# Optimization experiments

Hardware: AMD Instinct MI355X
Metric: run time of the kernel (lower is better)

## Reference

```python
import jax, jax.numpy as jnp
import numpy as np

RANK_WEIGHT = 0.1  # init kwarg rank_weight
EPS = 1e-08


def setup_inputs() -> dict:
    key = jax.random.key(0)
    k1, k2, k3, k4 = jax.random.split(key, 4)
    B, D = 8192, 128
    return {
        "q_embeddings": jax.random.normal(k1, (B, D), dtype=jnp.float32),
        "a_embeddings": jax.random.normal(k2, (B, D), dtype=jnp.float32),
        "question_ids": jax.random.randint(k3, (B,), 0, 2048, dtype=jnp.int64),
        "ranks": jax.random.uniform(k4, (B,), dtype=jnp.float32),
    }


def reference(q_embeddings, a_embeddings, question_ids, ranks):
    # NOTE: the original computes q@a.T/temperature into `similarity` but the
    # per-sample loop recomputes sims WITHOUT temperature; we match the loop math.
    sims = jnp.matmul(q_embeddings, a_embeddings.T)  # [B, B]
    same_q = question_ids[:, None] == question_ids[None, :]  # [B, B] bool
    # pos_mask weight per positive column j: 1 - rank_weight * ranks[j]
    w = jnp.where(same_q, 1.0 - RANK_WEIGHT * ranks[None, :], 0.0)  # [B, B]
    # stable exp-ratio: sum(w*exp(s)) / sum(exp(s))
    m = jnp.max(sims, axis=1, keepdims=True)
    e = jnp.exp(sims - m)
    num = jnp.sum(w * e, axis=1)
    den = jnp.sum(e, axis=1)
    loss = jnp.mean(-jnp.log(num / den + EPS))
    pred = jnp.argmax(sims, axis=1)  # [B]
    correct = jnp.take_along_axis(w, pred[:, None], axis=1)[:, 0] > 0
    accuracy = jnp.mean(correct.astype(jnp.float32))
    return loss, accuracy
```

## Files before the change

kernel.cpp:

```cpp
#include <hip/hip_runtime.h>
#include <hip/hip_bf16.h>
#include <cmath>

#define B_N 8192
#define D_K 128
#define CSPLIT 8
#define T_ITERS 16

typedef short bf16x8 __attribute__((ext_vector_type(8)));
typedef unsigned short u16x8 __attribute__((ext_vector_type(8)));
typedef float f32x4  __attribute__((ext_vector_type(4)));

__device__ inline unsigned short f2bf(float f) {
    unsigned u = __builtin_bit_cast(unsigned, f);
    u += 0x7fffu + ((u >> 16) & 1u);
    return (unsigned short)(u >> 16);
}

__global__ void cvt_kernel(const float* __restrict__ q, const float* __restrict__ a,
                           unsigned short* __restrict__ qb, unsigned short* __restrict__ ab,
                           float* __restrict__ out) {
    int g = blockIdx.x * blockDim.x + threadIdx.x;
    if (g < 2) out[g] = 0.0f;
    float4 q0 = reinterpret_cast<const float4*>(q)[g * 2];
    float4 q1 = reinterpret_cast<const float4*>(q)[g * 2 + 1];
    u16x8 oq;
    oq[0] = f2bf(q0.x); oq[1] = f2bf(q0.y); oq[2] = f2bf(q0.z); oq[3] = f2bf(q0.w);
    oq[4] = f2bf(q1.x); oq[5] = f2bf(q1.y); oq[6] = f2bf(q1.z); oq[7] = f2bf(q1.w);
    *reinterpret_cast<u16x8*>(qb + (size_t)g * 8) = oq;

    float4 a0 = reinterpret_cast<const float4*>(a)[g * 2];
    float4 a1 = reinterpret_cast<const float4*>(a)[g * 2 + 1];
    u16x8 oa;
    oa[0] = f2bf(a0.x); oa[1] = f2bf(a0.y); oa[2] = f2bf(a0.z); oa[3] = f2bf(a0.w);
    oa[4] = f2bf(a1.x); oa[5] = f2bf(a1.y); oa[6] = f2bf(a1.z); oa[7] = f2bf(a1.w);
    const int col = g >> 4, sq = g & 15, s = sq >> 2, quad = sq & 3;
    const int chunk = ((col >> 4) * 4 + s) * 64 + quad * 16 + (col & 15);
    *reinterpret_cast<u16x8*>(ab + (size_t)chunk * 8) = oa;
}

__launch_bounds__(256, 4)
__global__ void mpl_part_kernel(const unsigned short* __restrict__ qb,
                                const unsigned short* __restrict__ ab,
                                const int* __restrict__ qids,
                                const float* __restrict__ ranks,
                                float* __restrict__ pden, float* __restrict__ pnum,
                                float* __restrict__ pmax, float* __restrict__ pmaxp) {
    const int tid  = threadIdx.x;
    const int lane = tid & 63;
    const int wave = tid >> 6;
    const int rg   = blockIdx.x >> 3;
    const int cs   = blockIdx.x & 7;
    const int rowBase = rg * 32;
    const int quad = lane >> 4;
    const int l15  = lane & 15;

    bf16x8 qfrag[2][4];
    #pragma unroll
    for (int rt = 0; rt < 2; ++rt) {
        const unsigned short* qrow = qb + (size_t)(rowBase + rt * 16 + l15) * D_K + quad * 8;
        #pragma unroll
        for (int s = 0; s < 4; ++s)
            qfrag[rt][s] = *reinterpret_cast<const bf16x8*>(qrow + s * 32);
    }

    int qidrow[2][4];
    #pragma unroll
    for (int rt = 0; rt < 2; ++rt)
        #pragma unroll
        for (int r = 0; r < 4; ++r)
            qidrow[rt][r] = qids[rowBase + rt * 16 + quad * 4 + r];

    float den[2][4], num[2][4], mxv[2][4], mxp[2][4];
    #pragma unroll
    for (int rt = 0; rt < 2; ++rt)
        #pragma unroll
        for (int r = 0; r < 4; ++r) {
            den[rt][r] = 0.f; num[rt][r] = 0.f;
            mxv[rt][r] = -INFINITY; mxp[rt][r] = -INFINITY;
        }

    const float L2E = 1.4426950408889634f;
    const float CB  = 64.0f;

    const int colStart = cs * 1024 + wave * 256;
    const int tileBase = colStart >> 4;

    #pragma unroll 2
    for (int t = 0; t < T_ITERS; ++t) {
        const int c  = colStart + t * 16 + l15;
        const int qc = qids[c];
        const float wc = 1.0f - 0.1f * ranks[c];

        const unsigned short* bbase = ab + ((size_t)(tileBase + t) * 4) * 512 + lane * 8;
        bf16x8 bfrag[4];
        #pragma unroll
        for (int s = 0; s < 4; ++s)
            bfrag[s] = *reinterpret_cast<const bf16x8*>(bbase + s * 512);

        f32x4 acc0 = {0.f, 0.f, 0.f, 0.f};
        f32x4 acc1 = {0.f, 0.f, 0.f, 0.f};
        #pragma unroll
        for (int s = 0; s < 4; ++s) {
            acc0 = __builtin_amdgcn_mfma_f32_16x16x32_bf16(qfrag[0][s], bfrag[s], acc0, 0, 0, 0);
            acc1 = __builtin_amdgcn_mfma_f32_16x16x32_bf16(qfrag[1][s], bfrag[s], acc1, 0, 0, 0);
        }

        #pragma unroll
        for (int r = 0; r < 4; ++r) {
            {
                float sv = acc0[r];
                float e  = __builtin_amdgcn_exp2f(fmaf(sv, L2E, -CB));
                bool pos = (qc == qidrow[0][r]);
                den[0][r] += e;
                num[0][r] = fmaf(pos ? wc : 0.0f, e, num[0][r]);
                mxv[0][r] = fmaxf(mxv[0][r], sv);
                mxp[0][r] = fmaxf(mxp[0][r], pos ? sv : -INFINITY);
            }
            {
                float sv = acc1[r];
                float e  = __builtin_amdgcn_exp2f(fmaf(sv, L2E, -CB));
                bool pos = (qc == qidrow[1][r]);
                den[1][r] += e;
                num[1][r] = fmaf(pos ? wc : 0.0f, e, num[1][r]);
                mxv[1][r] = fmaxf(mxv[1][r], sv);
                mxp[1][r] = fmaxf(mxp[1][r], pos ? sv : -INFINITY);
            }
        }
    }

    #pragma unroll
    for (int m = 1; m <= 8; m <<= 1) {
        #pragma unroll
        for (int rt = 0; rt < 2; ++rt)
            #pragma unroll
            for (int r = 0; r < 4; ++r) {
                den[rt][r] += __shfl_xor(den[rt][r], m, 64);
                num[rt][r] += __shfl_xor(num[rt][r], m, 64);
                mxv[rt][r]  = fmaxf(mxv[rt][r], __shfl_xor(mxv[rt][r], m, 64));
                mxp[rt][r]  = fmaxf(mxp[rt][r], __shfl_xor(mxp[rt][r], m, 64));
            }
    }

    __shared__ float sden[4][32], snum[4][32], smax[4][32], smaxp[4][32];
    if (l15 == 0) {
        #pragma unroll
        for (int rt = 0; rt < 2; ++rt)
            #pragma unroll
            for (int r = 0; r < 4; ++r) {
                int lr = rt * 16 + quad * 4 + r;
                sden[wave][lr]  = den[rt][r];
                snum[wave][lr]  = num[rt][r];
                smax[wave][lr]  = mxv[rt][r];
                smaxp[wave][lr] = mxp[rt][r];
            }
    }
    __syncthreads();

    if (tid < 32) {
        int lr = tid;
        float d = 0.f, n = 0.f, mv = -INFINITY, mp = -INFINITY;
        #pragma unroll
        for (int w = 0; w < 4; ++w) {
            d += sden[w][lr];
            n += snum[w][lr];
            mv = fmaxf(mv, smax[w][lr]);
            mp = fmaxf(mp, smaxp[w][lr]);
        }
        const int row = rowBase + lr;
        pden[cs * B_N + row]  = d;
        pnum[cs * B_N + row]  = n;
        pmax[cs * B_N + row]  = mv;
        pmaxp[cs * B_N + row] = mp;
    }
}

__launch_bounds__(256, 4)
__global__ void fin_kernel(const float* __restrict__ pden, const float* __restrict__ pnum,
                           const float* __restrict__ pmax, const float* __restrict__ pmaxp,
                           float* __restrict__ out) {
    const int r = blockIdx.x * 256 + threadIdx.x;
    float d = 0.f, n = 0.f, mv = -INFINITY, mp = -INFINITY;
    #pragma unroll
    for (int cs = 0; cs < CSPLIT; ++cs) {
        d += pden[cs * B_N + r];
        n += pnum[cs * B_N + r];
        mv = fmaxf(mv, pmax[cs * B_N + r]);
        mp = fmaxf(mp, pmaxp[cs * B_N + r]);
    }
    float lsum = -logf(n / d + 1e-8f);
    float csum = (mp == mv) ? 1.0f : 0.0f;
    #pragma unroll
    for (int m = 1; m <= 32; m <<= 1) {
        lsum += __shfl_xor(lsum, m, 64);
        csum += __shfl_xor(csum, m, 64);
    }
    __shared__ float sl[4], sc[4];
    const int wave = threadIdx.x >> 6;
    if ((threadIdx.x & 63) == 0) { sl[wave] = lsum; sc[wave] = csum; }
    __syncthreads();
    if (threadIdx.x == 0) {
        float L = sl[0] + sl[1] + sl[2] + sl[3];
        float C = sc[0] + sc[1] + sc[2] + sc[3];
        atomicAdd(&out[0], L * (1.0f / B_N));
        atomicAdd(&out[1], C * (1.0f / B_N));
    }
}

extern "C" void kernel_launch(void* const* d_in, const int* in_sizes, int n_in,
                              void* d_out, int out_size, void* d_ws, size_t ws_size,
                              hipStream_t stream) {
    const float* q     = (const float*)d_in[0];
    const float* a     = (const float*)d_in[1];
    const int*   qids  = (const int*)d_in[2];
    const float* ranks = (const float*)d_in[3];
    float* out = (float*)d_out;

    unsigned short* qb = (unsigned short*)d_ws;
    unsigned short* ab = qb + (size_t)B_N * D_K;
    char* p = (char*)(ab + (size_t)B_N * D_K);
    float* pden  = (float*)p;                p += CSPLIT * B_N * sizeof(float);
    float* pnum  = (float*)p;                p += CSPLIT * B_N * sizeof(float);
    float* pmax  = (float*)p;                p += CSPLIT * B_N * sizeof(float);
    float* pmaxp = (float*)p;

    cvt_kernel<<<(B_N * D_K / 8) / 256, 256, 0, stream>>>(q, a, qb, ab, out);
    mpl_part_kernel<<<256 * CSPLIT, 256, 0, stream>>>(qb, ab, qids, ranks, pden, pnum, pmax, pmaxp);
    fin_kernel<<<B_N / 256, 256, 0, stream>>>(pden, pnum, pmax, pmaxp, out);
}
```

Baseline: 115.0 us.

## Switch matmul to FP8 MFMA and fuse final reduction via last-block counter

Converts q and a embeddings to FP8 (e4m3) packed fragments instead of bf16, halving operand bytes and using the fp8 MFMA instruction. The separate finalize kernel is removed: each block bumps an atomic counter, and the last block reduces all partials and writes loss and accuracy directly. This cuts one kernel launch and the memory traffic per operand, but FP8 precision may change argmax ties and the exp sums enough to affect accuracy and loss.

```diff
diff --git a/kernel.cpp b/kernel.cpp
--- a/kernel.cpp
+++ b/kernel.cpp
@@ -1,51 +1,55 @@
 #include <hip/hip_runtime.h>
-#include <hip/hip_bf16.h>
 #include <cmath>
 
 #define B_N 8192
 #define D_K 128
 #define CSPLIT 8
 #define T_ITERS 16
-
-typedef short bf16x8 __attribute__((ext_vector_type(8)));
-typedef unsigned short u16x8 __attribute__((ext_vector_type(8)));
-typedef float f32x4  __attribute__((ext_vector_type(4)));
-
-__device__ inline unsigned short f2bf(float f) {
-    unsigned u = __builtin_bit_cast(unsigned, f);
-    u += 0x7fffu + ((u >> 16) & 1u);
-    return (unsigned short)(u >> 16);
-}
+#define GRID_MPL (256 * CSPLIT)
+
+typedef float f32x4 __attribute__((ext_vector_type(4)));
+typedef long  lx2   __attribute__((ext_vector_type(2)));
 
 __global__ void cvt_kernel(const float* __restrict__ q, const float* __restrict__ a,
-                           unsigned short* __restrict__ qb, unsigned short* __restrict__ ab,
-                           float* __restrict__ out) {
-    int g = blockIdx.x * blockDim.x + threadIdx.x;
-    if (g < 2) out[g] = 0.0f;
+                           unsigned char* __restrict__ qp, unsigned char* __restrict__ ap,
+                           unsigned int* __restrict__ cnt) {
+    const int g = blockIdx.x * blockDim.x + threadIdx.x;
+    if (g == 0) *cnt = 0u;
+
     float4 q0 = reinterpret_cast<const float4*>(q)[g * 2];
     float4 q1 = reinterpret_cast<const float4*>(q)[g * 2 + 1];
-    u16x8 oq;
-    oq[0] = f2bf(q0.x); oq[1] = f2bf(q0.y); oq[2] = f2bf(q0.z); oq[3] = f2bf(q0.w);
-    oq[4] = f2bf(q1.x); oq[5] = f2bf(q1.y); oq[6] = f2bf(q1.z); oq[7] = f2bf(q1.w);
-    *reinterpret_cast<u16x8*>(qb + (size_t)g * 8) = oq;
-
     float4 a0 = reinterpret_cast<const float4*>(a)[g * 2];
     float4 a1 = reinterpret_cast<const float4*>(a)[g * 2 + 1];
-    u16x8 oa;
-    oa[0] = f2bf(a0.x); oa[1] = f2bf(a0.y); oa[2] = f2bf(a0.z); oa[3] = f2bf(a0.w);
-    oa[4] = f2bf(a1.x); oa[5] = f2bf(a1.y); oa[6] = f2bf(a1.z); oa[7] = f2bf(a1.w);
-    const int col = g >> 4, sq = g & 15, s = sq >> 2, quad = sq & 3;
-    const int chunk = ((col >> 4) * 4 + s) * 64 + quad * 16 + (col & 15);
-    *reinterpret_cast<u16x8*>(ab + (size_t)chunk * 8) = oa;
+
+    int qw0 = __builtin_amdgcn_cvt_pk_fp8_f32(q0.x, q0.y, 0, false);
+    qw0     = __builtin_amdgcn_cvt_pk_fp8_f32(q0.z, q0.w, qw0, true);
+    int qw1 = __builtin_amdgcn_cvt_pk_fp8_f32(q1.x, q1.y, 0, false);
+    qw1     = __builtin_amdgcn_cvt_pk_fp8_f32(q1.z, q1.w, qw1, true);
+    int aw0 = __builtin_amdgcn_cvt_pk_fp8_f32(a0.x, a0.y, 0, false);
+    aw0     = __builtin_amdgcn_cvt_pk_fp8_f32(a0.z, a0.w, aw0, true);
+    int aw1 = __builtin_amdgcn_cvt_pk_fp8_f32(a1.x, a1.y, 0, false);
+    aw1     = __builtin_amdgcn_cvt_pk_fp8_f32(a1.z, a1.w, aw1, true);
+
+    const int idx  = g >> 4;
+    const int sq   = g & 15;
+    const int s    = sq >> 2;
+    const int quad = sq & 3;
+    const int tile = idx >> 4, e = idx & 15;
+    const int lane = quad * 16 + e;
+    const size_t off = ((size_t)(tile * 2 + (s >> 1)) << 10) + (size_t)lane * 16 + (size_t)(s & 1) * 8;
+    *reinterpret_cast<int2*>(qp + off) = make_int2(qw0, qw1);
+    *reinterpret_cast<int2*>(ap + off) = make_int2(aw0, aw1);
 }
 
 __launch_bounds__(256, 4)
-__global__ void mpl_part_kernel(const unsigned short* __restrict__ qb,
-                                const unsigned short* __restrict__ ab,
-                                const int* __restrict__ qids,
-                                const float* __restrict__ ranks,
-                                float* __restrict__ pden, float* __restrict__ pnum,
-                                float* __restrict__ pmax, float* __restrict__ pmaxp) {
+__global__ void mpl_kernel(const unsigned char* __restrict__ qp,
+                           const unsigned char* __restrict__ ap,
+                           const int* __restrict__ qids,
+                           const float* __restrict__ ranks,
+                           float* __restrict__ pden, float* __restrict__ pnum,
+                           float* __restrict__ pmax, float* __restrict__ pmaxp,
+                           unsigned int* __restrict__ cnt,
+                           float* __restrict__ out) {
     const int tid  = threadIdx.x;
     const int lane = tid & 63;
     const int wave = tid >> 6;
@@ -55,13 +59,14 @@
     const int quad = lane >> 4;
     const int l15  = lane & 15;
 
-    bf16x8 qfrag[2][4];
+    long qfrag[2][4];
     #pragma unroll
     for (int rt = 0; rt < 2; ++rt) {
-        const unsigned short* qrow = qb + (size_t)(rowBase + rt * 16 + l15) * D_K + quad * 8;
-        #pragma unroll
-        for (int s = 0; s < 4; ++s)
-            qfrag[rt][s] = *reinterpret_cast<const bf16x8*>(qrow + s * 32);
+        const unsigned char* qbb = qp + ((size_t)((rowBase >> 4) + rt) << 11) + (size_t)lane * 16;
+        lx2 p0 = *reinterpret_cast<const lx2*>(qbb);
+        lx2 p1 = *reinterpret_cast<const lx2*>(qbb + 1024);
+        qfrag[rt][0] = p0[0]; qfrag[rt][1] = p0[1];
+        qfrag[rt][2] = p1[0]; qfrag[rt][3] = p1[1];
     }
 
     int qidrow[2][4];
@@ -92,18 +97,17 @@
         const int qc = qids[c];
         const float wc = 1.0f - 0.1f * ranks[c];
 
-        const unsigned short* bbase = ab + ((size_t)(tileBase + t) * 4) * 512 + lane * 8;
-        bf16x8 bfrag[4];
-        #pragma unroll
-        for (int s = 0; s < 4; ++s)
-            bfrag[s] = *reinterpret_cast<const bf16x8*>(bbase + s * 512);
+        const unsigned char* bb = ap + ((size_t)(tileBase + t) << 11) + (size_t)lane * 16;
+        lx2 b01 = *reinterpret_cast<const lx2*>(bb);
+        lx2 b23 = *reinterpret_cast<const lx2*>(bb + 1024);
+        long bfrag[4] = { b01[0], b01[1], b23[0], b23[1] };
 
         f32x4 acc0 = {0.f, 0.f, 0.f, 0.f};
         f32x4 acc1 = {0.f, 0.f, 0.f, 0.f};
         #pragma unroll
         for (int s = 0; s < 4; ++s) {
-            acc0 = __builtin_amdgcn_mfma_f32_16x16x32_bf16(qfrag[0][s], bfrag[s], acc0, 0, 0, 0);
-            acc1 = __builtin_amdgcn_mfma_f32_16x16x32_bf16(qfrag[1][s], bfrag[s], acc1, 0, 0, 0);
+            acc0 = __builtin_amdgcn_mfma_f32_16x16x32_fp8_fp8(qfrag[0][s], bfrag[s], acc0, 0, 0, 0);
+            acc1 = __builtin_amdgcn_mfma_f32_16x16x32_fp8_fp8(qfrag[1][s], bfrag[s], acc1, 0, 0, 0);
         }
 
         #pragma unroll
@@ -157,53 +161,66 @@
     }
     __syncthreads();
 
+    __shared__ int slast;
     if (tid < 32) {
-        int lr = tid;
         float d = 0.f, n = 0.f, mv = -INFINITY, mp = -INFINITY;
         #pragma unroll
         for (int w = 0; w < 4; ++w) {
-            d += sden[w][lr];
-            n += snum[w][lr];
-            mv = fmaxf(mv, smax[w][lr]);
-            mp = fmaxf(mp, smaxp[w][lr]);
-        }
-        const int row = rowBase + lr;
-        pden[cs * B_N + row]  = d;
-        pnum[cs * B_N + row]  = n;
-        pmax[cs * B_N + row]  = mv;
-        pmaxp[cs * B_N + row] = mp;
-    }
-}
-
-__launch_bounds__(256, 4)
-__global__ void fin_kernel(const float* __restrict__ pden, const float* __restrict__ pnum,
-                           const float* __restrict__ pmax, const float* __restrict__ pmaxp,
-                           float* __restrict__ out) {
-    const int r = blockIdx.x * 256 + threadIdx.x;
-    float d = 0.f, n = 0.f, mv = -INFINITY, mp = -INFINITY;
-    #pragma unroll
-    for (int cs = 0; cs < CSPLIT; ++cs) {
-        d += pden[cs * B_N + r];
-        n += pnum[cs * B_N + r];
-        mv = fmaxf(mv, pmax[cs * B_N + r]);
-        mp = fmaxf(mp, pmaxp[cs * B_N + r]);
-    }
-    float lsum = -logf(n / d + 1e-8f);
-    float csum = (mp == mv) ? 1.0f : 0.0f;
+            d += sden[w][tid];
+            n += snum[w][tid];
+            mv = fmaxf(mv, smax[w][tid]);
+            mp = fmaxf(mp, smaxp[w][tid]);
+        }
+        const int row = rowBase + tid;
+        __hip_atomic_store(&pden[cs * B_N + row],  d,  __ATOMIC_RELAXED, __HIP_MEMORY_SCOPE_AGENT);
+        __hip_atomic_store(&pnum[cs * B_N + row],  n,  __ATOMIC_RELAXED, __HIP_MEMORY_SCOPE_AGENT);
+        __hip_atomic_store(&pmax[cs * B_N + row],  mv, __ATOMIC_RELAXED, __HIP_MEMORY_SCOPE_AGENT);
+        __hip_atomic_store(&pmaxp[cs * B_N + row], mp, __ATOMIC_RELAXED, __HIP_MEMORY_SCOPE_AGENT);
+        if (tid == 0) {
+            __builtin_amdgcn_fence(__ATOMIC_RELEASE, "agent");
+            unsigned old = __hip_atomic_fetch_add(cnt, 1u, __ATOMIC_RELAXED, __HIP_MEMORY_SCOPE_AGENT);
+            slast = (old == GRID_MPL - 1) ? 1 : 0;
+        }
+    }
+    __syncthreads();
+    if (!slast) return;
+
+    __builtin_amdgcn_fence(__ATOMIC_ACQUIRE, "agent");
+    float lsum = 0.f, csum = 0.f;
+    for (int base = tid * 4; base < B_N; base += 1024) {
+        f32x4 d4 = {0.f, 0.f, 0.f, 0.f}, n4 = {0.f, 0.f, 0.f, 0.f};
+        f32x4 v4 = {-INFINITY, -INFINITY, -INFINITY, -INFINITY};
+        f32x4 p4 = {-INFINITY, -INFINITY, -INFINITY, -INFINITY};
+        #pragma unroll
+        for (int c2 = 0; c2 < CSPLIT; ++c2) {
+            const f32x4 dd = *reinterpret_cast<const f32x4*>(&pden[c2 * B_N + base]);
+            const f32x4 nn = *reinterpret_cast<const f32x4*>(&pnum[c2 * B_N + base]);
+            const f32x4 vv = *reinterpret_cast<const f32x4*>(&pmax[c2 * B_N + base]);
+            const f32x4 pp = *reinterpret_cast<const f32x4*>(&pmaxp[c2 * B_N + base]);
+            d4 += dd; n4 += nn;
+            #pragma unroll
+            for (int j = 0; j < 4; ++j) {
+                v4[j] = fmaxf(v4[j], vv[j]);
+                p4[j] = fmaxf(p4[j], pp[j]);
+            }
+        }
+        #pragma unroll
+        for (int j = 0; j < 4; ++j) {
+            lsum += -logf(n4[j] / d4[j] + 1e-8f);
+            csum += (p4[j] == v4[j]) ? 1.0f : 0.0f;
+        }
+    }
     #pragma unroll
     for (int m = 1; m <= 32; m <<= 1) {
         lsum += __shfl_xor(lsum, m, 64);
         csum += __shfl_xor(csum, m, 64);
     }
     __shared__ float sl[4], sc[4];
-    const int wave = threadIdx.x >> 6;
-    if ((threadIdx.x & 63) == 0) { sl[wave] = lsum; sc[wave] = csum; }
+    if ((tid & 63) == 0) { sl[wave] = lsum; sc[wave] = csum; }
     __syncthreads();
-    if (threadIdx.x == 0) {
-        float L = sl[0] + sl[1] + sl[2] + sl[3];
-        float C = sc[0] + sc[1] + sc[2] + sc[3];
-        atomicAdd(&out[0], L * (1.0f / B_N));
-        atomicAdd(&out[1], C * (1.0f / B_N));
+    if (tid == 0) {
+        out[0] = (sl[0] + sl[1] + sl[2] + sl[3]) * (1.0f / B_N);
+        out[1] = (sc[0] + sc[1] + sc[2] + sc[3]) * (1.0f / B_N);
     }
 }
 
@@ -216,15 +233,16 @@
     const float* ranks = (const float*)d_in[3];
     float* out = (float*)d_out;
 
-    unsigned short* qb = (unsigned short*)d_ws;
-    unsigned short* ab = qb + (size_t)B_N * D_K;
-    char* p = (char*)(ab + (size_t)B_N * D_K);
+    unsigned char* qp = (unsigned char*)d_ws;
+    unsigned char* ap = qp + (size_t)B_N * D_K;
+    char* p = (char*)(ap + (size_t)B_N * D_K);
     float* pden  = (float*)p;                p += CSPLIT * B_N * sizeof(float);
     float* pnum  = (float*)p;                p += CSPLIT * B_N * sizeof(float);
     float* pmax  = (float*)p;                p += CSPLIT * B_N * sizeof(float);
-    float* pmaxp = (float*)p;
-
-    cvt_kernel<<<(B_N * D_K / 8) / 256, 256, 0, stream>>>(q, a, qb, ab, out);
-    mpl_part_kernel<<<256 * CSPLIT, 256, 0, stream>>>(qb, ab, qids, ranks, pden, pnum, pmax, pmaxp);
-    fin_kernel<<<B_N / 256, 256, 0, stream>>>(pden, pnum, pmax, pmaxp, out);
+    float* pmaxp = (float*)p;                p += CSPLIT * B_N * sizeof(float);
+    unsigned int* cnt = (unsigned int*)p;
+
+    cvt_kernel<<<(B_N * D_K / 8) / 256, 256, 0, stream>>>(q, a, qp, ap, cnt);
+    mpl_kernel<<<GRID_MPL, 256, 0, stream>>>(qp, ap, qids, ranks,
+                                             pden, pnum, pmax, pmaxp, cnt, out);
 }
```

Result: slower. 131.2 us (+14.1%).

## Widen row tile to 64 rows per block and preload column ids via shuffles

Applied to the files above, without the earlier changes.

Each block now handles 64 query rows instead of 32, so every B fragment loaded from global memory feeds four MFMAs rather than two. This halves the total B-matrix traffic and the grid size. The per-column question ids and ranks are loaded once into registers up front and broadcast with lane shuffles, replacing a global load every iteration. The cost is more registers: launch bounds drop to 2 blocks per SM, which lowers occupancy and latency hiding.

```diff
diff --git a/kernel.cpp b/kernel.cpp
--- a/kernel.cpp
+++ b/kernel.cpp
@@ -4,6 +4,7 @@
 
 #define B_N 8192
 #define D_K 128
+#define ROWS 64
 #define CSPLIT 8
 #define T_ITERS 16
 
@@ -39,7 +40,7 @@
     *reinterpret_cast<u16x8*>(ab + (size_t)chunk * 8) = oa;
 }
 
-__launch_bounds__(256, 4)
+__launch_bounds__(256, 2)
 __global__ void mpl_part_kernel(const unsigned short* __restrict__ qb,
                                 const unsigned short* __restrict__ ab,
                                 const int* __restrict__ qids,
@@ -51,29 +52,38 @@
     const int wave = tid >> 6;
     const int rg   = blockIdx.x >> 3;
     const int cs   = blockIdx.x & 7;
-    const int rowBase = rg * 32;
+    const int rowBase = rg * ROWS;
     const int quad = lane >> 4;
     const int l15  = lane & 15;
 
-    bf16x8 qfrag[2][4];
-    #pragma unroll
-    for (int rt = 0; rt < 2; ++rt) {
+    bf16x8 qfrag[4][4];
+    #pragma unroll
+    for (int rt = 0; rt < 4; ++rt) {
         const unsigned short* qrow = qb + (size_t)(rowBase + rt * 16 + l15) * D_K + quad * 8;
         #pragma unroll
         for (int s = 0; s < 4; ++s)
             qfrag[rt][s] = *reinterpret_cast<const bf16x8*>(qrow + s * 32);
     }
 
-    int qidrow[2][4];
-    #pragma unroll
-    for (int rt = 0; rt < 2; ++rt)
+    int qidrow[4][4];
+    #pragma unroll
+    for (int rt = 0; rt < 4; ++rt)
         #pragma unroll
         for (int r = 0; r < 4; ++r)
             qidrow[rt][r] = qids[rowBase + rt * 16 + quad * 4 + r];
 
-    float den[2][4], num[2][4], mxv[2][4], mxp[2][4];
-    #pragma unroll
-    for (int rt = 0; rt < 2; ++rt)
+    const int colStart = cs * 1024 + wave * 256;
+    int   qreg[4];
+    float rreg[4];
+    #pragma unroll
+    for (int j = 0; j < 4; ++j) {
+        qreg[j] = qids[colStart + j * 64 + lane];
+        rreg[j] = ranks[colStart + j * 64 + lane];
+    }
+
+    float den[4][4], num[4][4], mxv[4][4], mxp[4][4];
+    #pragma unroll
+    for (int rt = 0; rt < 4; ++rt)
         #pragma unroll
         for (int r = 0; r < 4; ++r) {
             den[rt][r] = 0.f; num[rt][r] = 0.f;
@@ -82,15 +92,13 @@
 
     const float L2E = 1.4426950408889634f;
     const float CB  = 64.0f;
-
-    const int colStart = cs * 1024 + wave * 256;
     const int tileBase = colStart >> 4;
 
     #pragma unroll 2
     for (int t = 0; t < T_ITERS; ++t) {
-        const int c  = colStart + t * 16 + l15;
-        const int qc = qids[c];
-        const float wc = 1.0f - 0.1f * ranks[c];
+        const int   src = (t & 3) * 16 + l15;
+        const int   qc  = __shfl(qreg[t >> 2], src, 64);
+        const float wc  = 1.0f - 0.1f * __shfl(rreg[t >> 2], src, 64);
 
         const unsigned short* bbase = ab + ((size_t)(tileBase + t) * 4) * 512 + lane * 8;
         bf16x8 bfrag[4];
@@ -98,41 +106,33 @@
         for (int s = 0; s < 4; ++s)
             bfrag[s] = *reinterpret_cast<const bf16x8*>(bbase + s * 512);
 
-        f32x4 acc0 = {0.f, 0.f, 0.f, 0.f};
-        f32x4 acc1 = {0.f, 0.f, 0.f, 0.f};
-        #pragma unroll
-        for (int s = 0; s < 4; ++s) {
-            acc0 = __builtin_amdgcn_mfma_f32_16x16x32_bf16(qfrag[0][s], bfrag[s], acc0, 0, 0, 0);
-            acc1 = __builtin_amdgcn_mfma_f32_16x16x32_bf16(qfrag[1][s], bfrag[s], acc1, 0, 0, 0);
-        }
-
-        #pragma unroll
-        for (int r = 0; r < 4; ++r) {
-            {
-                float sv = acc0[r];
+        f32x4 acc[4];
+        #pragma unroll
+        for (int rt = 0; rt < 4; ++rt) acc[rt] = f32x4{0.f, 0.f, 0.f, 0.f};
+        #pragma unroll
+        for (int s = 0; s < 4; ++s)
+            #pragma unroll
+            for (int rt = 0; rt < 4; ++rt)
+                acc[rt] = __builtin_amdgcn_mfma_f32_16x16x32_bf16(qfrag[rt][s], bfrag[s], acc[rt], 0, 0, 0);
+
+        #pragma unroll
+        for (int rt = 0; rt < 4; ++rt)
+            #pragma unroll
+            for (int r = 0; r < 4; ++r) {
+                float sv = acc[rt][r];
                 float e  = __builtin_amdgcn_exp2f(fmaf(sv, L2E, -CB));
-                bool pos = (qc == qidrow[0][r]);
-                den[0][r] += e;
-                num[0][r] = fmaf(pos ? wc : 0.0f, e, num[0][r]);
-                mxv[0][r] = fmaxf(mxv[0][r], sv);
-                mxp[0][r] = fmaxf(mxp[0][r], pos ? sv : -INFINITY);
+                bool pos = (qc == qidrow[rt][r]);
+                den[rt][r] += e;
+                num[rt][r] = fmaf(pos ? wc : 0.0f, e, num[rt][r]);
+                mxv[rt][r] = fmaxf(mxv[rt][r], sv);
+                mxp[rt][r] = fmaxf(mxp[rt][r], pos ? sv : -INFINITY);
             }
-            {
-                float sv = acc1[r];
-                float e  = __builtin_amdgcn_exp2f(fmaf(sv, L2E, -CB));
-                bool pos = (qc == qidrow[1][r]);
-                den[1][r] += e;
-                num[1][r] = fmaf(pos ? wc : 0.0f, e, num[1][r]);
-                mxv[1][r] = fmaxf(mxv[1][r], sv);
-                mxp[1][r] = fmaxf(mxp[1][r], pos ? sv : -INFINITY);
-            }
-        }
     }
 
     #pragma unroll
     for (int m = 1; m <= 8; m <<= 1) {
         #pragma unroll
-        for (int rt = 0; rt < 2; ++rt)
+        for (int rt = 0; rt < 4; ++rt)
             #pragma unroll
             for (int r = 0; r < 4; ++r) {
                 den[rt][r] += __shfl_xor(den[rt][r], m, 64);
@@ -142,10 +142,10 @@
             }
     }
 
-    __shared__ float sden[4][32], snum[4][32], smax[4][32], smaxp[4][32];
+    __shared__ float sden[4][ROWS], snum[4][ROWS], smax[4][ROWS], smaxp[4][ROWS];
     if (l15 == 0) {
         #pragma unroll
-        for (int rt = 0; rt < 2; ++rt)
+        for (int rt = 0; rt < 4; ++rt)
             #pragma unroll
             for (int r = 0; r < 4; ++r) {
                 int lr = rt * 16 + quad * 4 + r;
@@ -157,7 +157,7 @@
     }
     __syncthreads();
 
-    if (tid < 32) {
+    if (tid < ROWS) {
         int lr = tid;
         float d = 0.f, n = 0.f, mv = -INFINITY, mp = -INFINITY;
         #pragma unroll
@@ -225,6 +225,7 @@
     float* pmaxp = (float*)p;
 
     cvt_kernel<<<(B_N * D_K / 8) / 256, 256, 0, stream>>>(q, a, qb, ab, out);
-    mpl_part_kernel<<<256 * CSPLIT, 256, 0, stream>>>(qb, ab, qids, ranks, pden, pnum, pmax, pmaxp);
+    mpl_part_kernel<<<(B_N / ROWS) * CSPLIT, 256, 0, stream>>>(qb, ab, qids, ranks,
+                                                               pden, pnum, pmax, pmaxp);
     fin_kernel<<<B_N / 256, 256, 0, stream>>>(pden, pnum, pmax, pmaxp, out);
 }
```

Measured after the change: 109.3 us. -5.0%, faster.

## Stage B tiles in LDS via async global_load_lds with double buffering

Applied to the files above, without the earlier changes.

Each block now covers 64 rows, one 16-row tile per wave, and all four waves share column tiles of the answer matrix. Those tiles are staged into LDS with asynchronous global-to-LDS loads and double buffered, so the next tile loads while MFMAs run on the current one. The aim is to cut redundant global reads of the B matrix and overlap load latency with compute. The cost is a block-wide barrier every iteration and 32KB of LDS per block, which halves the block count and may reduce occupancy.

```diff
diff --git a/kernel.cpp b/kernel.cpp
--- a/kernel.cpp
+++ b/kernel.cpp
@@ -4,12 +4,22 @@
 
 #define B_N 8192
 #define D_K 128
+#define ROWS 64
 #define CSPLIT 8
-#define T_ITERS 16
+#define T_OUT 16
 
 typedef short bf16x8 __attribute__((ext_vector_type(8)));
 typedef unsigned short u16x8 __attribute__((ext_vector_type(8)));
 typedef float f32x4  __attribute__((ext_vector_type(4)));
+
+typedef __attribute__((address_space(3))) unsigned int as3_uint;
+typedef __attribute__((address_space(1))) unsigned int as1_uint;
+
+__device__ __forceinline__ void gl_lds16(const void* g, void* l) {
+    __builtin_amdgcn_global_load_lds((const as1_uint*)(uintptr_t)g,
+                                     (as3_uint*)(unsigned int)(uintptr_t)l,
+                                     16, 0, 0);
+}
 
 __device__ inline unsigned short f2bf(float f) {
     unsigned u = __builtin_bit_cast(unsigned, f);
@@ -46,132 +56,110 @@
                                 const float* __restrict__ ranks,
                                 float* __restrict__ pden, float* __restrict__ pnum,
                                 float* __restrict__ pmax, float* __restrict__ pmaxp) {
+    __shared__ unsigned short smem[2 * 8192];
+
     const int tid  = threadIdx.x;
     const int lane = tid & 63;
     const int wave = tid >> 6;
     const int rg   = blockIdx.x >> 3;
     const int cs   = blockIdx.x & 7;
-    const int rowBase = rg * 32;
+    const int rowBase = rg * ROWS;
     const int quad = lane >> 4;
     const int l15  = lane & 15;
 
-    bf16x8 qfrag[2][4];
-    #pragma unroll
-    for (int rt = 0; rt < 2; ++rt) {
-        const unsigned short* qrow = qb + (size_t)(rowBase + rt * 16 + l15) * D_K + quad * 8;
+    bf16x8 qfrag[4];
+    {
+        const unsigned short* qrow = qb + (size_t)(rowBase + wave * 16 + l15) * D_K + quad * 8;
         #pragma unroll
         for (int s = 0; s < 4; ++s)
-            qfrag[rt][s] = *reinterpret_cast<const bf16x8*>(qrow + s * 32);
-    }
-
-    int qidrow[2][4];
-    #pragma unroll
-    for (int rt = 0; rt < 2; ++rt)
-        #pragma unroll
-        for (int r = 0; r < 4; ++r)
-            qidrow[rt][r] = qids[rowBase + rt * 16 + quad * 4 + r];
-
-    float den[2][4], num[2][4], mxv[2][4], mxp[2][4];
-    #pragma unroll
-    for (int rt = 0; rt < 2; ++rt)
-        #pragma unroll
-        for (int r = 0; r < 4; ++r) {
-            den[rt][r] = 0.f; num[rt][r] = 0.f;
-            mxv[rt][r] = -INFINITY; mxp[rt][r] = -INFINITY;
-        }
+            qfrag[s] = *reinterpret_cast<const bf16x8*>(qrow + s * 32);
+    }
+
+    int qidrow[4];
+    #pragma unroll
+    for (int r = 0; r < 4; ++r)
+        qidrow[r] = qids[rowBase + wave * 16 + quad * 4 + r];
+
+    float den[4], num[4], mxv[4], mxp[4];
+    #pragma unroll
+    for (int r = 0; r < 4; ++r) {
+        den[r] = 0.f; num[r] = 0.f; mxv[r] = -INFINITY; mxp[r] = -INFINITY;
+    }
 
     const float L2E = 1.4426950408889634f;
     const float CB  = 64.0f;
-
-    const int colStart = cs * 1024 + wave * 256;
-    const int tileBase = colStart >> 4;
-
-    #pragma unroll 2
-    for (int t = 0; t < T_ITERS; ++t) {
-        const int c  = colStart + t * 16 + l15;
-        const int qc = qids[c];
-        const float wc = 1.0f - 0.1f * ranks[c];
-
-        const unsigned short* bbase = ab + ((size_t)(tileBase + t) * 4) * 512 + lane * 8;
-        bf16x8 bfrag[4];
-        #pragma unroll
-        for (int s = 0; s < 4; ++s)
-            bfrag[s] = *reinterpret_cast<const bf16x8*>(bbase + s * 512);
-
-        f32x4 acc0 = {0.f, 0.f, 0.f, 0.f};
-        f32x4 acc1 = {0.f, 0.f, 0.f, 0.f};
-        #pragma unroll
-        for (int s = 0; s < 4; ++s) {
-            acc0 = __builtin_amdgcn_mfma_f32_16x16x32_bf16(qfrag[0][s], bfrag[s], acc0, 0, 0, 0);
-            acc1 = __builtin_amdgcn_mfma_f32_16x16x32_bf16(qfrag[1][s], bfrag[s], acc1, 0, 0, 0);
-        }
-
-        #pragma unroll
-        for (int r = 0; r < 4; ++r) {
-            {
-                float sv = acc0[r];
-                float e  = __builtin_amdgcn_exp2f(fmaf(sv, L2E, -CB));
-                bool pos = (qc == qidrow[0][r]);
-                den[0][r] += e;
-                num[0][r] = fmaf(pos ? wc : 0.0f, e, num[0][r]);
-                mxv[0][r] = fmaxf(mxv[0][r], sv);
-                mxp[0][r] = fmaxf(mxp[0][r], pos ? sv : -INFINITY);
+    const int colStart = cs * 1024;
+
+    const char* gstrip = (const char*)ab + (size_t)cs * 64 * 4096;
+    const int   chunk  = (wave * 4) * 1024;
+
+    #pragma unroll
+    for (int r = 0; r < 4; ++r)
+        gl_lds16(gstrip + chunk + r * 1024 + lane * 16,
+                 (char*)smem + chunk + r * 1024);
+    __syncthreads();
+
+    for (int t = 0; t < T_OUT; ++t) {
+        const int cur = t & 1, nxt = cur ^ 1;
+        if (t + 1 < T_OUT) {
+            const char* gsrc = gstrip + (size_t)(t + 1) * 16384 + chunk;
+            char*       ldst = (char*)smem + nxt * 16384 + chunk;
+            #pragma unroll
+            for (int r = 0; r < 4; ++r)
+                gl_lds16(gsrc + r * 1024 + lane * 16, ldst + r * 1024);
+        }
+
+        const unsigned short* lbase = smem + cur * 8192 + lane * 8;
+        f32x4 acc[4];
+        #pragma unroll
+        for (int u = 0; u < 4; ++u) acc[u] = f32x4{0.f, 0.f, 0.f, 0.f};
+        #pragma unroll
+        for (int u = 0; u < 4; ++u)
+            #pragma unroll
+            for (int s = 0; s < 4; ++s) {
+                bf16x8 bfrag = *reinterpret_cast<const bf16x8*>(lbase + u * 2048 + s * 512);
+                acc[u] = __builtin_amdgcn_mfma_f32_16x16x32_bf16(qfrag[s], bfrag, acc[u], 0, 0, 0);
             }
-            {
-                float sv = acc1[r];
-                float e  = __builtin_amdgcn_exp2f(fmaf(sv, L2E, -CB));
-                bool pos = (qc == qidrow[1][r]);
-                den[1][r] += e;
-                num[1][r] = fmaf(pos ? wc : 0.0f, e, num[1][r]);
-                mxv[1][r] = fmaxf(mxv[1][r], sv);
-                mxp[1][r] = fmaxf(mxp[1][r], pos ? sv : -INFINITY);
-            }
-        }
-    }
-
-    #pragma unroll
-    for (int m = 1; m <= 8; m <<= 1) {
-        #pragma unroll
-        for (int rt = 0; rt < 2; ++rt)
+
+        #pragma unroll
+        for (int u = 0; u < 4; ++u) {
+            const int c  = colStart + t * 64 + u * 16 + l15;
+            const int qc = qids[c];
+            const float wc = 1.0f - 0.1f * ranks[c];
             #pragma unroll
             for (int r = 0; r < 4; ++r) {
-                den[rt][r] += __shfl_xor(den[rt][r], m, 64);
-                num[rt][r] += __shfl_xor(num[rt][r], m, 64);
-                mxv[rt][r]  = fmaxf(mxv[rt][r], __shfl_xor(mxv[rt][r], m, 64));
-                mxp[rt][r]  = fmaxf(mxp[rt][r], __shfl_xor(mxp[rt][r], m, 64));
+                float sv = acc[u][r];
+                float e  = __builtin_amdgcn_exp2f(fmaf(sv, L2E, -CB));
+                bool pos = (qc == qidrow[r]);
+                den[r] += e;
+                num[r] = fmaf(pos ? wc : 0.0f, e, num[r]);
+                mxv[r] = fmaxf(mxv[r], sv);
+                mxp[r] = fmaxf(mxp[r], pos ? sv : -INFINITY);
             }
-    }
-
-    __shared__ float sden[4][32], snum[4][32], smax[4][32], smaxp[4][32];
+        }
+        __syncthreads();
+    }
+
+    #pragma unroll
+    for (int m = 1; m <= 8; m <<= 1) {
+        #pragma unroll
+        for (int r = 0; r < 4; ++r) {
+            den[r] += __shfl_xor(den[r], m, 64);
+            num[r] += __shfl_xor(num[r], m, 64);
+            mxv[r]  = fmaxf(mxv[r], __shfl_xor(mxv[r], m, 64));
+            mxp[r]  = fmaxf(mxp[r], __shfl_xor(mxp[r], m, 64));
+        }
+    }
+
     if (l15 == 0) {
-        #pragma unroll
-        for (int rt = 0; rt < 2; ++rt)
-            #pragma unroll
-            for (int r = 0; r < 4; ++r) {
-                int lr = rt * 16 + quad * 4 + r;
-                sden[wave][lr]  = den[rt][r];
-                snum[wave][lr]  = num[rt][r];
-                smax[wave][lr]  = mxv[rt][r];
-                smaxp[wave][lr] = mxp[rt][r];
-            }
-    }
-    __syncthreads();
-
-    if (tid < 32) {
-        int lr = tid;
-        float d = 0.f, n = 0.f, mv = -INFINITY, mp = -INFINITY;
-        #pragma unroll
-        for (int w = 0; w < 4; ++w) {
-            d += sden[w][lr];
-            n += snum[w][lr];
-            mv = fmaxf(mv, smax[w][lr]);
-            mp = fmaxf(mp, smaxp[w][lr]);
-        }
-        const int row = rowBase + lr;
-        pden[cs * B_N + row]  = d;
-        pnum[cs * B_N + row]  = n;
-        pmax[cs * B_N + row]  = mv;
-        pmaxp[cs * B_N + row] = mp;
+        const int rb = cs * B_N + rowBase + wave * 16 + quad * 4;
+        #pragma unroll
+        for (int r = 0; r < 4; ++r) {
+            pden[rb + r]  = den[r];
+            pnum[rb + r]  = num[r];
+            pmax[rb + r]  = mxv[r];
+            pmaxp[rb + r] = mxp[r];
+        }
     }
 }
 
@@ -225,6 +213,7 @@
     float* pmaxp = (float*)p;
 
     cvt_kernel<<<(B_N * D_K / 8) / 256, 256, 0, stream>>>(q, a, qb, ab, out);
-    mpl_part_kernel<<<256 * CSPLIT, 256, 0, stream>>>(qb, ab, qids, ranks, pden, pnum, pmax, pmaxp);
+    mpl_part_kernel<<<(B_N / ROWS) * CSPLIT, 256, 0, stream>>>(qb, ab, qids, ranks,
+                                                               pden, pnum, pmax, pmaxp);
     fin_kernel<<<B_N / 256, 256, 0, stream>>>(pden, pnum, pmax, pmaxp, out);
 }
```

New measurement: 99.82 us. 13.2% less time.
